# Performance work log

Hardware: AMD Instinct MI355X
Metric: run time of the kernel (lower is better)

## Reference

```python
import jax, jax.numpy as jnp
import numpy as np

SCALE = 256 ** -0.5  # d_proj ** -0.5

def setup_inputs() -> dict:
    key = jax.random.key(0)
    k1, k2, k3, k4 = jax.random.split(key, 4)
    B, L, T = 8, 2048, 512
    Dh, Dg, Dp = 1024, 768, 256
    H = jax.random.normal(k1, (B, L, Dh), dtype=jnp.float32)
    G = jax.random.normal(k2, (B, T, Dg), dtype=jnp.float32)
    mask = jnp.zeros((B, L), dtype=jnp.int32)  # True/nonzero = masked OUT
    Wk = jax.random.normal(k3, (Dh, Dp), dtype=jnp.float32) * (Dh ** -0.5)
    Wq = jax.random.normal(k4, (Dg, Dp), dtype=jnp.float32) * (Dg ** -0.5)
    return {"H": H, "G": G, "mask": mask, "Wk": Wk, "Wq": Wq}

def reference(H, G, mask, Wk, Wq):
    # K: [B,L,Dp], Q: [B,T,Dp]
    K = jnp.einsum('bld,dp->blp', H, Wk)
    Q = jnp.einsum('btd,dp->btp', G, Wq)
    # logits over keys L: [B,T,L]
    logits = jnp.einsum('btp,blp->btl', Q, K) * SCALE
    logits = jnp.where(mask[:, None, :] != 0, -jnp.inf, logits)
    alpha = jax.nn.softmax(logits, axis=-1)  # online-softmax in torch == exact softmax
    Z = jnp.einsum('btl,bld->btd', alpha, H)  # [B,T,Dh]
    return Z
```

## Files before the change

kernel.cpp:

```cpp
#include <hip/hip_runtime.h>
#include <math.h>

#define BATCH 8
#define LKEYS 2048
#define TQ    512
#define DH    1024
#define DG    768
#define DP    256
#define SCALE 0.0625f

typedef short  short8  __attribute__((ext_vector_type(8)));
typedef float  floatx4 __attribute__((ext_vector_type(4)));
typedef unsigned short u16x4 __attribute__((ext_vector_type(4)));
typedef unsigned short u16x8 __attribute__((ext_vector_type(8)));

typedef unsigned int __attribute__((address_space(1))) as1_uint;
typedef unsigned int __attribute__((address_space(3))) as3_uint;

__device__ __forceinline__ unsigned short f2b(float f) {
    union { float f; unsigned int u; } v; v.f = f;
    unsigned int u = v.u;
    unsigned int r = u + 0x7fffu + ((u >> 16) & 1u);
    if ((u & 0x7f800000u) == 0x7f800000u) r = u;
    return (unsigned short)(r >> 16);
}
__device__ __forceinline__ float b2f(unsigned short b) {
    union { unsigned int u; float f; } v; v.u = ((unsigned int)b) << 16;
    return v.f;
}

__device__ __forceinline__ void gload_lds16(const void* g, void* l) {
    __builtin_amdgcn_global_load_lds((const as1_uint*)g, (as3_uint*)l, 16, 0, 0);
}

__host__ __device__ constexpr int wcnt_vm(int vm) {
    return (vm & 15) | ((vm >> 4) << 14) | (7 << 4) | (15 << 8);
}

template<int BM, int BN, int OMODE, int SWZ, int KS>
__global__ __launch_bounds__(256) void gemm_bf16_p(
    const unsigned short* __restrict__ Ap, const unsigned short* __restrict__ Bp,
    const int* __restrict__ maskp, void* __restrict__ Cp,
    int K, int lda, int ldb, int ldc,
    long sA, long sB, long sC, long sM, long sP, float scale)
{
    constexpr int FM = BM / 32, FN = BN / 32;
    constexpr int AI = BM / 64, BI = BN / 64;
    constexpr int NL = AI + BI;

    __shared__ unsigned short As[4][BM * 32];
    __shared__ unsigned short Bs[4][BN * 32];

    int bx = blockIdx.x, by = blockIdx.y, zz = blockIdx.z;
    if (SWZ == 1) {
        const int gx = gridDim.x;
        const int nwg = gx * gridDim.y;
        const int f = by * gx + bx;
        const int nper = nwg >> 3;
        const int fl = (f & 7) * nper + (f >> 3);
        bx = fl % gx; by = fl / gx;
    } else if (SWZ == 2) {
        const int gx = gridDim.x, nxy = gridDim.x * gridDim.y;
        const long l = blockIdx.x + (long)gx * (blockIdx.y + (long)gridDim.y * blockIdx.z);
        const int xcd  = (int)(l & 7);
        const int slot = (int)(l >> 3);
        zz = xcd + 8 * (slot / nxy);
        const int rem = slot % nxy;
        bx = rem % gx; by = rem / gx;
    }
    const int z    = (KS > 1) ? (zz & 7) : zz;
    const int part = (KS > 1) ? (zz >> 3) : 0;
    const int koff = part * K;

    const int tid  = threadIdx.x;
    const int lane = tid & 63;
    const int wid  = tid >> 6;
    const int wr   = wid >> 1, wc = wid & 1;
    const int lrow = lane & 15;
    const int g    = lane >> 4;

    const unsigned short* A = Ap + (long)z * sA + (long)(by * BM) * lda + koff;
    const unsigned short* B = Bp + (long)z * sB + (long)(bx * BN) * ldb + koff;
    const int srow = tid >> 2, sslot = tid & 3;

    const int nt = K / 32;
    floatx4 acc[FM][FN] = {};

    auto stage = [&](int t, int b) {
        const int k0 = t * 32;
        #pragma unroll
        for (int i = 0; i < AI; ++i)
            gload_lds16(A + (long)(srow + i * 64) * lda + k0 + sslot * 8,
                        (void*)&As[b][(i * 256 + tid) * 8]);
        #pragma unroll
        for (int i = 0; i < BI; ++i)
            gload_lds16(B + (long)(srow + i * 64) * ldb + k0 + sslot * 8,
                        (void*)&Bs[b][(i * 256 + tid) * 8]);
    };

    stage(0, 0);
    stage(1, 1);
    for (int t = 0; t < nt; ++t) {
        if (t + 2 < nt) {
            stage(t + 2, (t + 2) & 3);
            __builtin_amdgcn_s_waitcnt(wcnt_vm(2 * NL));
        } else if (t + 1 < nt) {
            __builtin_amdgcn_s_waitcnt(wcnt_vm(NL));
        } else {
            __builtin_amdgcn_s_waitcnt(wcnt_vm(0));
        }
        __builtin_amdgcn_s_barrier();
        __builtin_amdgcn_sched_barrier(0);

        const int b = t & 3;
        short8 a[FM], bf[FN];
        #pragma unroll
        for (int m = 0; m < FM; ++m)
            a[m] = *(const short8*)&As[b][(wr * (BM / 2) + m * 16 + lrow) * 32 + g * 8];
        #pragma unroll
        for (int n = 0; n < FN; ++n)
            bf[n] = *(const short8*)&Bs[b][(wc * (BN / 2) + n * 16 + lrow) * 32 + g * 8];
        __builtin_amdgcn_s_setprio(1);
        #pragma unroll
        for (int m = 0; m < FM; ++m)
            #pragma unroll
            for (int n = 0; n < FN; ++n)
                acc[m][n] = __builtin_amdgcn_mfma_f32_16x16x32_bf16(
                    a[m], bf[n], acc[m][n], 0, 0, 0);
        __builtin_amdgcn_s_setprio(0);
        __builtin_amdgcn_sched_barrier(0);
    }

    const int orow = by * BM + wr * (BM / 2);
    const int ocol = bx * BN + wc * (BN / 2);
    if (OMODE == 0) {
        float* C = (float*)Cp + (long)z * sC + (long)part * sP;
        #pragma unroll
        for (int m = 0; m < FM; ++m)
            #pragma unroll
            for (int n = 0; n < FN; ++n)
                #pragma unroll
                for (int r = 0; r < 4; ++r)
                    C[(long)(orow + m * 16 + 4 * g + r) * ldc + ocol + n * 16 + lrow]
                        = acc[m][n][r];
    } else if (OMODE == 1) {
        unsigned short* C = (unsigned short*)Cp + (long)z * sC + (long)part * sP;
        #pragma unroll
        for (int m = 0; m < FM; ++m)
            #pragma unroll
            for (int n = 0; n < FN; ++n)
                #pragma unroll
                for (int r = 0; r < 4; ++r)
                    C[(long)(orow + m * 16 + 4 * g + r) * ldc + ocol + n * 16 + lrow]
                        = f2b(acc[m][n][r]);
    } else if (OMODE == 2) {
        const int* mask = maskp + (long)z * sM;
        float* C = (float*)Cp + (long)z * sC;
        #pragma unroll
        for (int n = 0; n < FN; ++n) {
            int c = ocol + n * 16 + lrow;
            bool masked = (mask[c] != 0);
            #pragma unroll
            for (int m = 0; m < FM; ++m)
                #pragma unroll
                for (int r = 0; r < 4; ++r)
                    C[(long)(orow + m * 16 + 4 * g + r) * ldc + c]
                        = masked ? -INFINITY : acc[m][n][r] * scale;
        }
    } else {
        const int* mask = maskp + (long)z * sM;
        unsigned short* C = (unsigned short*)Cp + (long)z * sC;
        #pragma unroll
        for (int n = 0; n < FN; ++n) {
            int c = ocol + n * 16 + lrow;
            bool masked = (mask[c] != 0);
            #pragma unroll
            for (int m = 0; m < FM; ++m)
                #pragma unroll
                for (int r = 0; r < 4; ++r)
                    C[(long)(orow + m * 16 + 4 * g + r) * ldc + c]
                        = masked ? (unsigned short)0xFF80u
                                 : f2b(acc[m][n][r] * scale);
        }
    }
}

#define NPROJ 640

__global__ __launch_bounds__(256) void proj_kq_ht(
    const unsigned short* __restrict__ Hb, const unsigned short* __restrict__ WkT,
    unsigned short* __restrict__ Kb,
    const unsigned short* __restrict__ Gb, const unsigned short* __restrict__ WqT,
    unsigned short* __restrict__ Qb,
    unsigned short* __restrict__ HbT)
{
    __shared__ unsigned short smem[4 * 128 * 32 + 4 * 64 * 32];
    const int tid = threadIdx.x;

    if (blockIdx.x >= NPROJ) {
        auto ts = (unsigned short(*)[68])smem;
        const int b  = blockIdx.x - NPROJ;
        const int z  = b >> 9;
        const int r_ = b & 511;
        const int l0 = (r_ >> 4) << 6;
        const int d0 = (r_ & 15) << 6;
        const unsigned short* Hz = Hb + (long)z * LKEYS * DH;
        unsigned short* Tz = HbT + (long)z * DH * LKEYS;
        #pragma unroll
        for (int j = 0; j < 4; ++j) {
            int idx = tid + j * 256, r = idx >> 4, c4 = idx & 15;
            *(u16x4*)&ts[r][4 * c4] = *(const u16x4*)&Hz[(long)(l0 + r) * DH + d0 + 4 * c4];
        }
        __syncthreads();
        #pragma unroll
        for (int j = 0; j < 4; ++j) {
            int idx = tid + j * 256, r = idx >> 4, c4 = idx & 15;
            u16x4 o;
            o[0] = ts[4 * c4 + 0][r]; o[1] = ts[4 * c4 + 1][r];
            o[2] = ts[4 * c4 + 2][r]; o[3] = ts[4 * c4 + 3][r];
            *(u16x4*)&Tz[(long)(d0 + r) * LKEYS + l0 + 4 * c4] = o;
        }
        return;
    }

    constexpr int FM = 4, FN = 2, AI = 2, NL = 3;
    auto As = (unsigned short(*)[128 * 32])smem;
    auto Bs = (unsigned short(*)[64 * 32])(smem + 4 * 128 * 32);

    const int f  = blockIdx.x;
    const int fl = (f & 7) * 80 + (f >> 3);
    const int bx = fl & 3, by = fl >> 2;

    const unsigned short *A, *B;
    unsigned short* C;
    int K, ld;
    if (by < 128) { A = Hb + (long)by * 128 * DH;          B = WkT; C = Kb; K = DH; ld = DH; }
    else          { A = Gb + (long)(by - 128) * 128 * DG;  B = WqT; C = Qb; K = DG; ld = DG; }
    B += (long)bx * 64 * ld;
    const int orow0 = (by < 128) ? by * 128 : (by - 128) * 128;

    const int lane = tid & 63;
    const int wid  = tid >> 6;
    const int wr   = wid >> 1, wc = wid & 1;
    const int lrow = lane & 15;
    const int g    = lane >> 4;
    const int srow = tid >> 2, sslot = tid & 3;

    const int nt = K / 32;
    floatx4 acc[FM][FN] = {};

    auto stage = [&](int t, int b) {
        const int k0 = t * 32;
        #pragma unroll
        for (int i = 0; i < AI; ++i)
            gload_lds16(A + (long)(srow + i * 64) * ld + k0 + sslot * 8,
                        (void*)&As[b][(i * 256 + tid) * 8]);
        gload_lds16(B + (long)srow * ld + k0 + sslot * 8,
                    (void*)&Bs[b][tid * 8]);
    };

    stage(0, 0);
    stage(1, 1);
    for (int t = 0; t < nt; ++t) {
        if (t + 2 < nt) {
            stage(t + 2, (t + 2) & 3);
            __builtin_amdgcn_s_waitcnt(wcnt_vm(2 * NL));
        } else if (t + 1 < nt) {
            __builtin_amdgcn_s_waitcnt(wcnt_vm(NL));
        } else {
            __builtin_amdgcn_s_waitcnt(wcnt_vm(0));
        }
        __builtin_amdgcn_s_barrier();
        __builtin_amdgcn_sched_barrier(0);

        const int b = t & 3;
        short8 a[FM], bf[FN];
        #pragma unroll
        for (int m = 0; m < FM; ++m)
            a[m] = *(const short8*)&As[b][(wr * 64 + m * 16 + lrow) * 32 + g * 8];
        #pragma unroll
        for (int n = 0; n < FN; ++n)
            bf[n] = *(const short8*)&Bs[b][(wc * 32 + n * 16 + lrow) * 32 + g * 8];
        __builtin_amdgcn_s_setprio(1);
        #pragma unroll
        for (int m = 0; m < FM; ++m)
            #pragma unroll
            for (int n = 0; n < FN; ++n)
                acc[m][n] = __builtin_amdgcn_mfma_f32_16x16x32_bf16(
                    a[m], bf[n], acc[m][n], 0, 0, 0);
        __builtin_amdgcn_s_setprio(0);
        __builtin_amdgcn_sched_barrier(0);
    }

    const int orow = orow0 + wr * 64;
    const int ocol = bx * 64 + wc * 32;
    #pragma unroll
    for (int m = 0; m < FM; ++m)
        #pragma unroll
        for (int n = 0; n < FN; ++n)
            #pragma unroll
            for (int r = 0; r < 4; ++r)
                C[(long)(orow + m * 16 + 4 * g + r) * DP + ocol + n * 16 + lrow]
                    = f2b(acc[m][n][r]);
}

#define NHS_BLK 8192
#define NG_BLK  1536
#define NWK_BLK 256
#define NWQ_BLK 192

__global__ __launch_bounds__(256) void prep_all(
    const float* __restrict__ H, const float* __restrict__ G,
    const float* __restrict__ Wk, const float* __restrict__ Wq,
    unsigned short* __restrict__ Hb, unsigned short* __restrict__ Gb,
    unsigned short* __restrict__ WkT, unsigned short* __restrict__ WqT)
{
    __shared__ float tf[32][33];
    const int id = blockIdx.x;

    if (id < NHS_BLK + NG_BLK) {
        const float* src; unsigned short* dst; long base;
        if (id < NHS_BLK) { src = H; dst = Hb; base = (long)id * 2048; }
        else              { src = G; dst = Gb; base = (long)(id - NHS_BLK) * 2048; }
        long i = base + (long)threadIdx.x * 8;
        float4 a = *(const float4*)&src[i];
        float4 b = *(const float4*)&src[i + 4];
        u16x8 w;
        w[0] = f2b(a.x); w[1] = f2b(a.y); w[2] = f2b(a.z); w[3] = f2b(a.w);
        w[4] = f2b(b.x); w[5] = f2b(b.y); w[6] = f2b(b.z); w[7] = f2b(b.w);
        *(u16x8*)&dst[i] = w;
    } else {
        const float* W; unsigned short* WT; int D, d0, p0;
        if (id < NHS_BLK + NG_BLK + NWK_BLK) {
            const int bid = id - NHS_BLK - NG_BLK;
            W = Wk; WT = WkT; D = DH;
            d0 = (bid & 31) * 32; p0 = (bid >> 5) * 32;
        } else {
            const int bid = id - NHS_BLK - NG_BLK - NWK_BLK;
            W = Wq; WT = WqT; D = DG;
            d0 = (bid % 24) * 32; p0 = (bid / 24) * 32;
        }
        const int tx = threadIdx.x & 31, ty = threadIdx.x >> 5;
        #pragma unroll
        for (int j = 0; j < 4; ++j)
            tf[ty + 8 * j][tx] = W[(long)(d0 + ty + 8 * j) * DP + p0 + tx];
        __syncthreads();
        #pragma unroll
        for (int j = 0; j < 4; ++j)
            WT[(long)(p0 + ty + 8 * j) * D + d0 + tx] = f2b(tf[tx][ty + 8 * j]);
    }
}

__global__ __launch_bounds__(256) void reduce_add2(
    const unsigned short* __restrict__ P, long sP, float* __restrict__ Zo)
{
    long i = ((long)blockIdx.x * 256 + threadIdx.x) * 8;
    u16x8 a = *(const u16x8*)&P[i];
    u16x8 b = *(const u16x8*)&P[i + sP];
    float4 o0, o1;
    o0.x = b2f(a[0]) + b2f(b[0]);
    o0.y = b2f(a[1]) + b2f(b[1]);
    o0.z = b2f(a[2]) + b2f(b[2]);
    o0.w = b2f(a[3]) + b2f(b[3]);
    o1.x = b2f(a[4]) + b2f(b[4]);
    o1.y = b2f(a[5]) + b2f(b[5]);
    o1.z = b2f(a[6]) + b2f(b[6]);
    o1.w = b2f(a[7]) + b2f(b[7]);
    *(float4*)&Zo[i] = o0;
    *(float4*)&Zo[i + 4] = o1;
}

__global__ __launch_bounds__(256) void softmax_kernel(
    const unsigned short* __restrict__ S, unsigned short* __restrict__ Ab)
{
    const u16x8* row8 = (const u16x8*)(S + (long)blockIdx.x * LKEYS);
    u16x8* out8 = (u16x8*)(Ab + (long)blockIdx.x * LKEYS);
    const int tid = threadIdx.x;
    __shared__ float red[4];

    u16x8 v = row8[tid];
    float x[8];
    #pragma unroll
    for (int j = 0; j < 8; ++j) x[j] = b2f(v[j]);

    float m = fmaxf(fmaxf(fmaxf(x[0], x[1]), fmaxf(x[2], x[3])),
                    fmaxf(fmaxf(x[4], x[5]), fmaxf(x[6], x[7])));
    #pragma unroll
    for (int off = 32; off > 0; off >>= 1) m = fmaxf(m, __shfl_xor(m, off));
    if ((tid & 63) == 0) red[tid >> 6] = m;
    __syncthreads();
    m = fmaxf(fmaxf(red[0], red[1]), fmaxf(red[2], red[3]));

    float e[8], s = 0.f;
    #pragma unroll
    for (int j = 0; j < 8; ++j) { e[j] = __expf(x[j] - m); s += e[j]; }
    #pragma unroll
    for (int off = 32; off > 0; off >>= 1) s += __shfl_xor(s, off);
    __syncthreads();
    if ((tid & 63) == 0) red[tid >> 6] = s;
    __syncthreads();
    s = red[0] + red[1] + red[2] + red[3];

    float inv = 1.0f / s;
    u16x8 o;
    #pragma unroll
    for (int j = 0; j < 8; ++j) o[j] = f2b(e[j] * inv);
    out8[tid] = o;
}

extern "C" void kernel_launch(void* const* d_in, const int* in_sizes, int n_in,
                              void* d_out, int out_size, void* d_ws, size_t ws_size,
                              hipStream_t stream)
{
    const float* H    = (const float*)d_in[0];
    const float* G    = (const float*)d_in[1];
    const int*   mask = (const int*)  d_in[2];
    const float* Wk   = (const float*)d_in[3];
    const float* Wq   = (const float*)d_in[4];
    float*       Z    = (float*)d_out;

    unsigned short* WkT = (unsigned short*)d_ws;
    unsigned short* WqT = WkT + 262144;
    unsigned short* Ab  = WqT + 196608;
    unsigned short* Kb  = Ab  + 8388608;
    unsigned short* Qb  = Kb  + 4194304;
    unsigned short* Gb  = Qb  + 1048576;
    unsigned short* HbT = Gb  + 3145728;
    unsigned short* Hb  = HbT + 16777216;
    unsigned short* S   = Hb;
    unsigned short* Zp  = Hb;
    const long sZp = (long)BATCH * TQ * DH;
    const long sZb = (long)TQ * DH;

    prep_all<<<NHS_BLK + NG_BLK + NWK_BLK + NWQ_BLK, 256, 0, stream>>>(
        H, G, Wk, Wq, Hb, Gb, WkT, WqT);

    proj_kq_ht<<<NPROJ + 4096, 256, 0, stream>>>(Hb, WkT, Kb, Gb, WqT, Qb, HbT);

    gemm_bf16_p<128, 128, 3, 2, 1><<<dim3(16, 4, BATCH), 256, 0, stream>>>(
        Qb, Kb, mask, S, DP, DP, DP, LKEYS,
        (long)TQ * DP, (long)LKEYS * DP, (long)TQ * LKEYS, (long)LKEYS, 0, SCALE);

    softmax_kernel<<<BATCH * TQ, 256, 0, stream>>>(S, Ab);

    gemm_bf16_p<128, 128, 1, 2, 2><<<dim3(8, 4, 2 * BATCH), 256, 0, stream>>>(
        Ab, HbT, nullptr, Zp, LKEYS / 2, LKEYS, LKEYS, DH,
        (long)TQ * LKEYS, (long)DH * LKEYS, sZb, 0, sZp, 1.f);

    reduce_add2<<<(int)(sZp / 8 / 256), 256, 0, stream>>>(Zp, sZp, Z);
}
```

Baseline: 101.6 us.

## Split-K the PV GEMM four ways and add a 3-buffer pipeline variant

The alpha·H GEMM now splits the key dimension into four parts instead of two, so the grid is twice as large. A four-way reduce kernel sums the partial results. A new PIPE=2 mode uses three LDS buffers and issues the next-next stage after the barrier, which lowers LDS use and may raise occupancy. In exchange there is more partial-result traffic through workspace (Zp aliases the Hb region), which risks overflowing it, and each block has a shorter K loop.

```diff
diff --git a/kernel.cpp b/kernel.cpp
--- a/kernel.cpp
+++ b/kernel.cpp
@@ -37,7 +37,7 @@
     return (vm & 15) | ((vm >> 4) << 14) | (7 << 4) | (15 << 8);
 }
 
-template<int BM, int BN, int OMODE, int SWZ, int KS>
+template<int BM, int BN, int OMODE, int SWZ, int KS, int PIPE>
 __global__ __launch_bounds__(256) void gemm_bf16_p(
     const unsigned short* __restrict__ Ap, const unsigned short* __restrict__ Bp,
     const int* __restrict__ maskp, void* __restrict__ Cp,
@@ -47,9 +47,10 @@
     constexpr int FM = BM / 32, FN = BN / 32;
     constexpr int AI = BM / 64, BI = BN / 64;
     constexpr int NL = AI + BI;
-
-    __shared__ unsigned short As[4][BM * 32];
-    __shared__ unsigned short Bs[4][BN * 32];
+    constexpr int NB = (PIPE == 2) ? 3 : 4;
+
+    __shared__ unsigned short As[NB][BM * 32];
+    __shared__ unsigned short Bs[NB][BN * 32];
 
     int bx = blockIdx.x, by = blockIdx.y, zz = blockIdx.z;
     if (SWZ == 1) {
@@ -98,21 +99,7 @@
                         (void*)&Bs[b][(i * 256 + tid) * 8]);
     };
 
-    stage(0, 0);
-    stage(1, 1);
-    for (int t = 0; t < nt; ++t) {
-        if (t + 2 < nt) {
-            stage(t + 2, (t + 2) & 3);
-            __builtin_amdgcn_s_waitcnt(wcnt_vm(2 * NL));
-        } else if (t + 1 < nt) {
-            __builtin_amdgcn_s_waitcnt(wcnt_vm(NL));
-        } else {
-            __builtin_amdgcn_s_waitcnt(wcnt_vm(0));
-        }
-        __builtin_amdgcn_s_barrier();
-        __builtin_amdgcn_sched_barrier(0);
-
-        const int b = t & 3;
+    auto compute = [&](int b) {
         short8 a[FM], bf[FN];
         #pragma unroll
         for (int m = 0; m < FM; ++m)
@@ -129,6 +116,36 @@
                     a[m], bf[n], acc[m][n], 0, 0, 0);
         __builtin_amdgcn_s_setprio(0);
         __builtin_amdgcn_sched_barrier(0);
+    };
+
+    if (PIPE == 0) {
+        stage(0, 0);
+        stage(1, 1);
+        for (int t = 0; t < nt; ++t) {
+            if (t + 2 < nt) {
+                stage(t + 2, (t + 2) & 3);
+                __builtin_amdgcn_s_waitcnt(wcnt_vm(2 * NL));
+            } else if (t + 1 < nt) {
+                __builtin_amdgcn_s_waitcnt(wcnt_vm(NL));
+            } else {
+                __builtin_amdgcn_s_waitcnt(wcnt_vm(0));
+            }
+            __builtin_amdgcn_s_barrier();
+            __builtin_amdgcn_sched_barrier(0);
+            compute(t & 3);
+        }
+    } else {
+        stage(0, 0);
+        stage(1, 1);
+        for (int t = 0; t < nt; ++t) {
+            if (t + 1 < nt) __builtin_amdgcn_s_waitcnt(wcnt_vm(NL));
+            else            __builtin_amdgcn_s_waitcnt(wcnt_vm(0));
+            __builtin_amdgcn_s_barrier();
+            __builtin_amdgcn_sched_barrier(0);
+            if (t + 2 < nt) stage(t + 2, (t + 2) % 3);
+            __builtin_amdgcn_sched_barrier(0);
+            compute(t % 3);
+        }
     }
 
     const int orow = by * BM + wr * (BM / 2);
@@ -351,21 +368,23 @@
     }
 }
 
-__global__ __launch_bounds__(256) void reduce_add2(
+__global__ __launch_bounds__(256) void reduce_add4(
     const unsigned short* __restrict__ P, long sP, float* __restrict__ Zo)
 {
     long i = ((long)blockIdx.x * 256 + threadIdx.x) * 8;
     u16x8 a = *(const u16x8*)&P[i];
     u16x8 b = *(const u16x8*)&P[i + sP];
+    u16x8 c = *(const u16x8*)&P[i + 2 * sP];
+    u16x8 d = *(const u16x8*)&P[i + 3 * sP];
     float4 o0, o1;
-    o0.x = b2f(a[0]) + b2f(b[0]);
-    o0.y = b2f(a[1]) + b2f(b[1]);
-    o0.z = b2f(a[2]) + b2f(b[2]);
-    o0.w = b2f(a[3]) + b2f(b[3]);
-    o1.x = b2f(a[4]) + b2f(b[4]);
-    o1.y = b2f(a[5]) + b2f(b[5]);
-    o1.z = b2f(a[6]) + b2f(b[6]);
-    o1.w = b2f(a[7]) + b2f(b[7]);
+    o0.x = (b2f(a[0]) + b2f(b[0])) + (b2f(c[0]) + b2f(d[0]));
+    o0.y = (b2f(a[1]) + b2f(b[1])) + (b2f(c[1]) + b2f(d[1]));
+    o0.z = (b2f(a[2]) + b2f(b[2])) + (b2f(c[2]) + b2f(d[2]));
+    o0.w = (b2f(a[3]) + b2f(b[3])) + (b2f(c[3]) + b2f(d[3]));
+    o1.x = (b2f(a[4]) + b2f(b[4])) + (b2f(c[4]) + b2f(d[4]));
+    o1.y = (b2f(a[5]) + b2f(b[5])) + (b2f(c[5]) + b2f(d[5]));
+    o1.z = (b2f(a[6]) + b2f(b[6])) + (b2f(c[6]) + b2f(d[6]));
+    o1.w = (b2f(a[7]) + b2f(b[7])) + (b2f(c[7]) + b2f(d[7]));
     *(float4*)&Zo[i] = o0;
     *(float4*)&Zo[i + 4] = o1;
 }
@@ -437,15 +456,15 @@
 
     proj_kq_ht<<<NPROJ + 4096, 256, 0, stream>>>(Hb, WkT, Kb, Gb, WqT, Qb, HbT);
 
-    gemm_bf16_p<128, 128, 3, 2, 1><<<dim3(16, 4, BATCH), 256, 0, stream>>>(
+    gemm_bf16_p<128, 128, 3, 2, 1, 0><<<dim3(16, 4, BATCH), 256, 0, stream>>>(
         Qb, Kb, mask, S, DP, DP, DP, LKEYS,
         (long)TQ * DP, (long)LKEYS * DP, (long)TQ * LKEYS, (long)LKEYS, 0, SCALE);
 
     softmax_kernel<<<BATCH * TQ, 256, 0, stream>>>(S, Ab);
 
-    gemm_bf16_p<128, 128, 1, 2, 2><<<dim3(8, 4, 2 * BATCH), 256, 0, stream>>>(
-        Ab, HbT, nullptr, Zp, LKEYS / 2, LKEYS, LKEYS, DH,
+    gemm_bf16_p<128, 128, 1, 2, 4, 2><<<dim3(8, 4, 4 * BATCH), 256, 0, stream>>>(
+        Ab, HbT, nullptr, Zp, LKEYS / 4, LKEYS, LKEYS, DH,
         (long)TQ * LKEYS, (long)DH * LKEYS, sZb, 0, sZp, 1.f);
 
-    reduce_add2<<<(int)(sZp / 8 / 256), 256, 0, stream>>>(Zp, sZp, Z);
-}
+    reduce_add4<<<(int)(sZp / 8 / 256), 256, 0, stream>>>(Zp, sZp, Z);
+}
```

Measured after the change: 109.7 us. +8.0%, slower.
